# Kernel optimization log

Hardware: AMD Instinct MI355X
Metric: run time of the kernel (lower is better)

## Reference

```python
import jax, jax.numpy as jnp
import numpy as np

N = 10000      # nodes (= num_spatial_nodes)
E = 320000     # edges
IN = 4         # in_channels
HID = 256      # hidden_channels
H1, C1 = 4, 64 # conv1: heads, per-head out (hidden//heads)
EDIM = 1       # edge_feature_size
EPS = 1e-5


def _layernorm(x, g, b):
    mu = jnp.mean(x, axis=-1, keepdims=True)
    var = jnp.mean(jnp.square(x - mu), axis=-1, keepdims=True)
    return (x - mu) / jnp.sqrt(var + EPS) * g + b


def _gatv2(x, src, dst, ea, Wl, bl, Wr, br, We, att, bias, H, C, n):
    # PyG GATv2Conv: lin_l on source, lin_r on target, lin_edge on edge_attr
    xl = (x @ Wl + bl).reshape(n, H, C)
    xr = (x @ Wr + br).reshape(n, H, C)
    ee = (ea @ We).reshape(-1, H, C)
    m = jax.nn.leaky_relu(xl[src] + xr[dst] + ee, 0.2)   # [E', H, C]
    logit = jnp.einsum('ehc,hc->eh', m, att)             # [E', H]
    # segment softmax over incoming edges of each dst node
    mx = jax.ops.segment_max(logit, dst, num_segments=n)
    ex = jnp.exp(logit - mx[dst])
    den = jax.ops.segment_sum(ex, dst, num_segments=n)
    alpha = ex / den[dst]
    out = jax.ops.segment_sum(xl[src] * alpha[:, :, None], dst, num_segments=n)
    return out.reshape(n, H * C) + bias


def setup_inputs() -> dict:
    key = jax.random.key(0)
    ks = jax.random.split(key, 32)
    gl = lambda k, shape, fan: (jax.random.normal(k, shape, jnp.float32) / np.sqrt(fan)).astype(jnp.float32)
    inp = {}
    inp['x'] = jax.random.normal(ks[0], (N, IN), jnp.float32)
    inp['edge_index'] = jax.random.randint(ks[1], (2, E), 0, N, jnp.int32)
    inp['edge_attr'] = jax.random.normal(ks[2], (E, EDIM), jnp.float32)
    # conv1 (heads=4, out=64, concat -> 256)
    inp['Wl1'] = gl(ks[3], (IN, HID), IN);  inp['bl1'] = jnp.zeros((HID,), jnp.float32)
    inp['Wr1'] = gl(ks[4], (IN, HID), IN);  inp['br1'] = jnp.zeros((HID,), jnp.float32)
    inp['We1'] = gl(ks[5], (EDIM, HID), EDIM)
    inp['att1'] = gl(ks[6], (H1, C1), C1)
    inp['bias1'] = jnp.zeros((HID,), jnp.float32)
    inp['g1'] = jnp.ones((HID,), jnp.float32); inp['be1'] = jnp.zeros((HID,), jnp.float32)
    # conv2 (heads=1, out=256)
    inp['Wl2'] = gl(ks[7], (HID, HID), HID); inp['bl2'] = jnp.zeros((HID,), jnp.float32)
    inp['Wr2'] = gl(ks[8], (HID, HID), HID); inp['br2'] = jnp.zeros((HID,), jnp.float32)
    inp['We2'] = gl(ks[9], (EDIM, HID), EDIM)
    inp['att2'] = gl(ks[10], (1, HID), HID)
    inp['bias2'] = jnp.zeros((HID,), jnp.float32)
    inp['g2'] = jnp.ones((HID,), jnp.float32); inp['be2'] = jnp.zeros((HID,), jnp.float32)
    # policy head
    inp['Wp1'] = gl(ks[11], (HID, HID // 2), HID); inp['bp1'] = jnp.zeros((HID // 2,), jnp.float32)
    inp['Wp2'] = gl(ks[12], (HID // 2, IN), HID // 2); inp['bp2'] = jnp.zeros((IN,), jnp.float32)
    return inp


def reference(x, edge_index, edge_attr,
              Wl1, bl1, Wr1, br1, We1, att1, bias1, g1, be1,
              Wl2, bl2, Wr2, br2, We2, att2, bias2, g2, be2,
              Wp1, bp1, Wp2, bp2):
    src, dst = edge_index[0], edge_index[1]
    # add_self_loops with fill_value='mean': loop edge_attr = mean of incoming edge_attr
    deg = jax.ops.segment_sum(jnp.ones((E,), jnp.float32), dst, num_segments=N)
    loop_attr = jax.ops.segment_sum(edge_attr, dst, num_segments=N) / jnp.maximum(deg, 1.0)[:, None]
    ar = jnp.arange(N, dtype=src.dtype)
    src_a = jnp.concatenate([src, ar]); dst_a = jnp.concatenate([dst, ar])
    ea_a = jnp.concatenate([edge_attr, loop_attr], axis=0)
    h = _gatv2(x, src_a, dst_a, ea_a, Wl1, bl1, Wr1, br1, We1, att1, bias1, H1, C1, N)
    h = jax.nn.relu(_layernorm(h, g1, be1))
    h = _gatv2(h, src_a, dst_a, ea_a, Wl2, bl2, Wr2, br2, We2, att2, bias2, 1, HID, N)
    h = jax.nn.relu(_layernorm(h, g2, be2))
    logits = jax.nn.relu(h @ Wp1 + bp1) @ Wp2 + bp2   # [N, IN]
    return jax.nn.softmax(logits.reshape(1, -1), axis=1)
```

## Files before the change

kernel.cpp:

```cpp
#include <hip/hip_runtime.h>
#include <math.h>

#define N_NODES 10000
#define N_EDGES 320000
#define N_AUG   (N_EDGES + N_NODES)
#define HID     256

typedef short short8 __attribute__((ext_vector_type(8)));
typedef float floatx16 __attribute__((ext_vector_type(16)));

static __device__ __forceinline__ unsigned bf16rne(float f) {
  unsigned u = __float_as_uint(f);
  return (u + 0x7FFFu + ((u >> 16) & 1u)) >> 16;
}

__global__ void k_deg(const int* __restrict__ dst, const float* __restrict__ ea,
                      int* __restrict__ deg, float* __restrict__ asum) {
  int e = blockIdx.x * blockDim.x + threadIdx.x;
  if (e < N_EDGES) {
    int d = dst[e];
    atomicAdd(&deg[d], 1);
    atomicAdd(&asum[d], ea[e]);
  }
}

__global__ void __launch_bounds__(256) k_scan(
    const int* __restrict__ deg, const float* __restrict__ asum,
    int* __restrict__ offs, float* __restrict__ lattr) {
  __shared__ int wsum[4];
  int t = threadIdx.x;
  int base = t * 40;
  int s = 0;
  for (int i = 0; i < 40; i++) {
    int n = base + i;
    if (n < N_NODES) s += deg[n] + 1;
  }
  int v = s;
  #pragma unroll
  for (int d = 1; d < 64; d <<= 1) {
    int u = __shfl_up(v, d);
    if ((t & 63) >= d) v += u;
  }
  if ((t & 63) == 63) wsum[t >> 6] = v;
  __syncthreads();
  int wb = 0;
  for (int i = 0; i < (t >> 6); i++) wb += wsum[i];
  int run = wb + v - s;
  for (int i = 0; i < 40; i++) {
    int n = base + i;
    if (n < N_NODES) {
      offs[n] = run;
      int d = deg[n];
      run += d + 1;
      lattr[n] = asum[n] / (float)max(d, 1);
    }
  }
  if (t == 255) offs[N_NODES] = wb + v;
}

__global__ void k_scatter(const int* __restrict__ src, const int* __restrict__ dst,
                          const float* __restrict__ ea, const float* __restrict__ lattr,
                          const int* __restrict__ offs, int* __restrict__ cursor,
                          int2* __restrict__ cpk) {
  int e = blockIdx.x * blockDim.x + threadIdx.x;
  if (e >= N_AUG) return;
  int s, d; float a;
  if (e < N_EDGES) { s = src[e]; d = dst[e]; a = ea[e]; }
  else             { s = e - N_EDGES; d = s; a = lattr[s]; }
  int pos = offs[d] + atomicAdd(&cursor[d], 1);
  cpk[pos] = make_int2(s, __float_as_int(a));
}

__global__ void __launch_bounds__(256) k_cvtw(
    const float* __restrict__ W1, const float* __restrict__ W2,
    unsigned short* __restrict__ Wt) {
  __shared__ float tile[32][33];
  const float* W = blockIdx.z ? W2 : W1;
  int rowoff = blockIdx.z * 256;
  int kb = blockIdx.x * 32, nb = blockIdx.y * 32;
  int t = threadIdx.x;
  int tx = t & 31, ty = t >> 5;
  #pragma unroll
  for (int rep = 0; rep < 4; rep++)
    tile[ty + 8*rep][tx] = W[(kb + ty + 8*rep)*HID + nb + tx];
  __syncthreads();
  #pragma unroll
  for (int rep = 0; rep < 4; rep++) {
    int n = nb + ty + 8*rep;
    Wt[(rowoff + n)*256 + kb + tx] = (unsigned short)bf16rne(tile[tx][ty + 8*rep]);
  }
}

__global__ void __launch_bounds__(256) k_cvtwp(
    const float* __restrict__ Wp1, unsigned short* __restrict__ Wp1t) {
  __shared__ float tile[32][33];
  int kb = blockIdx.x * 32, nb = blockIdx.y * 32;
  int t = threadIdx.x;
  int tx = t & 31, ty = t >> 5;
  #pragma unroll
  for (int rep = 0; rep < 4; rep++)
    tile[ty + 8*rep][tx] = Wp1[(kb + ty + 8*rep)*128 + nb + tx];
  __syncthreads();
  #pragma unroll
  for (int rep = 0; rep < 4; rep++) {
    int n = nb + ty + 8*rep;
    Wp1t[n*256 + kb + tx] = (unsigned short)bf16rne(tile[tx][ty + 8*rep]);
  }
}

#define C1_EDGE(xs, av, l0, l1, l2, l3, p)                                              \
  {                                                                                     \
    l0 = fmaf(xs.x,wl0.x, fmaf(xs.y,wl1.x, fmaf(xs.z,wl2.x, fmaf(xs.w,wl3.x, blv.x)))); \
    l1 = fmaf(xs.x,wl0.y, fmaf(xs.y,wl1.y, fmaf(xs.z,wl2.y, fmaf(xs.w,wl3.y, blv.y)))); \
    l2 = fmaf(xs.x,wl0.z, fmaf(xs.y,wl1.z, fmaf(xs.z,wl2.z, fmaf(xs.w,wl3.z, blv.z)))); \
    l3 = fmaf(xs.x,wl0.w, fmaf(xs.y,wl1.w, fmaf(xs.z,wl2.w, fmaf(xs.w,wl3.w, blv.w)))); \
    float m0 = l0 + fmaf(av, we.x, r4.x); m0 = fmaxf(m0, 0.2f*m0);                      \
    float m1 = l1 + fmaf(av, we.y, r4.y); m1 = fmaxf(m1, 0.2f*m1);                      \
    float m2 = l2 + fmaf(av, we.z, r4.z); m2 = fmaxf(m2, 0.2f*m2);                      \
    float m3 = l3 + fmaf(av, we.w, r4.w); m3 = fmaxf(m3, 0.2f*m3);                      \
    p = m0*at.x + m1*at.y + m2*at.z + m3*at.w;                                          \
  }

#define C1_PROC8()                                                              \
  {                                                                             \
    float4 xA = *(const float4*)&x[eA.x*4];                                     \
    float4 xB = *(const float4*)&x[eB.x*4];                                     \
    float4 xC = *(const float4*)&x[eC.x*4];                                     \
    float4 xD = *(const float4*)&x[eD.x*4];                                     \
    float4 xE = *(const float4*)&x[eE.x*4];                                     \
    float4 xF = *(const float4*)&x[eF.x*4];                                     \
    float4 xG = *(const float4*)&x[eG.x*4];                                     \
    float4 xH = *(const float4*)&x[eH.x*4];                                     \
    float avA = __int_as_float(eA.y), avB = __int_as_float(eB.y);               \
    float avC = __int_as_float(eC.y), avD = __int_as_float(eD.y);               \
    float avE = __int_as_float(eE.y), avF = __int_as_float(eF.y);               \
    float avG = __int_as_float(eG.y), avH = __int_as_float(eH.y);               \
    float lA0,lA1,lA2,lA3,pA, lB0,lB1,lB2,lB3,pB;                               \
    float lC0,lC1,lC2,lC3,pC, lD0,lD1,lD2,lD3,pD;                               \
    float lE0,lE1,lE2,lE3,pE, lF0,lF1,lF2,lF3,pF;                               \
    float lG0,lG1,lG2,lG3,pG, lH0,lH1,lH2,lH3,pH;                               \
    C1_EDGE(xA, avA, lA0,lA1,lA2,lA3, pA);                                      \
    C1_EDGE(xB, avB, lB0,lB1,lB2,lB3, pB);                                      \
    C1_EDGE(xC, avC, lC0,lC1,lC2,lC3, pC);                                      \
    C1_EDGE(xD, avD, lD0,lD1,lD2,lD3, pD);                                      \
    C1_EDGE(xE, avE, lE0,lE1,lE2,lE3, pE);                                      \
    C1_EDGE(xF, avF, lF0,lF1,lF2,lF3, pF);                                      \
    C1_EDGE(xG, avG, lG0,lG1,lG2,lG3, pG);                                      \
    C1_EDGE(xH, avH, lH0,lH1,lH2,lH3, pH);                                      \
    _Pragma("unroll")                                                           \
    for (int msk = 1; msk < 16; msk <<= 1) {                                    \
      pA += __shfl_xor(pA, msk); pB += __shfl_xor(pB, msk);                     \
      pC += __shfl_xor(pC, msk); pD += __shfl_xor(pD, msk);                     \
      pE += __shfl_xor(pE, msk); pF += __shfl_xor(pF, msk);                     \
      pG += __shfl_xor(pG, msk); pH += __shfl_xor(pH, msk);                     \
    }                                                                           \
    float eAx = expf(pA), eBx = expf(pB), eCx = expf(pC), eDx = expf(pD);       \
    float eEx = expf(pE), eFx = expf(pF), eGx = expf(pG), eHx = expf(pH);       \
    D += ((eAx + eBx) + (eCx + eDx)) + ((eEx + eFx) + (eGx + eHx));             \
    a0 = fmaf(eDx, lD0, fmaf(eCx, lC0, fmaf(eBx, lB0, fmaf(eAx, lA0, a0))));    \
    a0 = fmaf(eHx, lH0, fmaf(eGx, lG0, fmaf(eFx, lF0, fmaf(eEx, lE0, a0))));    \
    a1 = fmaf(eDx, lD1, fmaf(eCx, lC1, fmaf(eBx, lB1, fmaf(eAx, lA1, a1))));    \
    a1 = fmaf(eHx, lH1, fmaf(eGx, lG1, fmaf(eFx, lF1, fmaf(eEx, lE1, a1))));    \
    a2 = fmaf(eDx, lD2, fmaf(eCx, lC2, fmaf(eBx, lB2, fmaf(eAx, lA2, a2))));    \
    a2 = fmaf(eHx, lH2, fmaf(eGx, lG2, fmaf(eFx, lF2, fmaf(eEx, lE2, a2))));    \
    a3 = fmaf(eDx, lD3, fmaf(eCx, lC3, fmaf(eBx, lB3, fmaf(eAx, lA3, a3))));    \
    a3 = fmaf(eHx, lH3, fmaf(eGx, lG3, fmaf(eFx, lF3, fmaf(eEx, lE3, a3))));    \
  }

__global__ void __launch_bounds__(256) k_conv1(
    const float* __restrict__ x,
    const float* __restrict__ Wl, const float* __restrict__ bl,
    const float* __restrict__ Wr, const float* __restrict__ br,
    const float* __restrict__ We, const float* __restrict__ att,
    const int* __restrict__ offs, const int2* __restrict__ cpk,
    const float* __restrict__ bias, const float* __restrict__ g,
    const float* __restrict__ be, uint2* __restrict__ h1b) {
  int t = threadIdx.x;
  int n = blockIdx.x * 4 + (t >> 6);
  int c = 4 * (t & 63);

  float4 wl0 = *(const float4*)&Wl[0*HID + c];
  float4 wl1 = *(const float4*)&Wl[1*HID + c];
  float4 wl2 = *(const float4*)&Wl[2*HID + c];
  float4 wl3 = *(const float4*)&Wl[3*HID + c];
  float4 blv = *(const float4*)&bl[c];
  float4 we  = *(const float4*)&We[c];
  float4 at  = *(const float4*)&att[c];

  float4 xn = *(const float4*)&x[n*4];
  float4 r4;
  {
    float4 wr0 = *(const float4*)&Wr[0*HID + c];
    float4 wr1 = *(const float4*)&Wr[1*HID + c];
    float4 wr2 = *(const float4*)&Wr[2*HID + c];
    float4 wr3 = *(const float4*)&Wr[3*HID + c];
    float4 brv = *(const float4*)&br[c];
    r4.x = fmaf(xn.x,wr0.x, fmaf(xn.y,wr1.x, fmaf(xn.z,wr2.x, fmaf(xn.w,wr3.x, brv.x))));
    r4.y = fmaf(xn.x,wr0.y, fmaf(xn.y,wr1.y, fmaf(xn.z,wr2.y, fmaf(xn.w,wr3.y, brv.y))));
    r4.z = fmaf(xn.x,wr0.z, fmaf(xn.y,wr1.z, fmaf(xn.z,wr2.z, fmaf(xn.w,wr3.z, brv.z))));
    r4.w = fmaf(xn.x,wr0.w, fmaf(xn.y,wr1.w, fmaf(xn.z,wr2.w, fmaf(xn.w,wr3.w, brv.w))));
  }

  int js = __builtin_amdgcn_readfirstlane(offs[n]);
  int je = __builtin_amdgcn_readfirstlane(offs[n+1]);

  float D = 0.f, a0 = 0.f, a1 = 0.f, a2 = 0.f, a3 = 0.f;

  int j = js;
  if (j + 7 < je) {
    int2 eA = cpk[j],   eB = cpk[j+1], eC = cpk[j+2], eD = cpk[j+3];
    int2 eE = cpk[j+4], eF = cpk[j+5], eG = cpk[j+6], eH = cpk[j+7];
    for (; j + 7 < je; j += 8) {
      int2 nA = cpk[j+8],  nB = cpk[j+9],  nC = cpk[j+10], nD = cpk[j+11];
      int2 nE = cpk[j+12], nF = cpk[j+13], nG = cpk[j+14], nH = cpk[j+15];
      C1_PROC8();
      eA = nA; eB = nB; eC = nC; eD = nD;
      eE = nE; eF = nF; eG = nG; eH = nH;
    }
  }
  for (; j < je; j++) {
    int2 eA = cpk[j];
    float4 xA = *(const float4*)&x[eA.x*4];
    float avA = __int_as_float(eA.y);
    float lA0,lA1,lA2,lA3,pA;
    C1_EDGE(xA, avA, lA0,lA1,lA2,lA3, pA);
    #pragma unroll
    for (int msk = 1; msk < 16; msk <<= 1) pA += __shfl_xor(pA, msk);
    float eAx = expf(pA);
    D += eAx;
    a0 = fmaf(eAx, lA0, a0);
    a1 = fmaf(eAx, lA1, a1);
    a2 = fmaf(eAx, lA2, a2);
    a3 = fmaf(eAx, lA3, a3);
  }

  float inv = 1.f / D;
  float4 b4 = *(const float4*)&bias[c];
  float o0 = fmaf(a0, inv, b4.x);
  float o1 = fmaf(a1, inv, b4.y);
  float o2 = fmaf(a2, inv, b4.z);
  float o3 = fmaf(a3, inv, b4.w);

  float s = o0 + o1 + o2 + o3;
  #pragma unroll
  for (int msk = 1; msk < 64; msk <<= 1) s += __shfl_xor(s, msk);
  float mu = s * (1.f / 256.f);
  float d0 = o0 - mu, d1 = o1 - mu, d2 = o2 - mu, d3 = o3 - mu;
  float sq = d0*d0 + d1*d1 + d2*d2 + d3*d3;
  #pragma unroll
  for (int msk = 1; msk < 64; msk <<= 1) sq += __shfl_xor(sq, msk);
  float rstd = rsqrtf(sq * (1.f / 256.f) + 1e-5f);
  float4 g4  = *(const float4*)&g[c];
  float4 be4 = *(const float4*)&be[c];
  float oy0 = fmaxf(fmaf(d0 * rstd, g4.x, be4.x), 0.f);
  float oy1 = fmaxf(fmaf(d1 * rstd, g4.y, be4.y), 0.f);
  float oy2 = fmaxf(fmaf(d2 * rstd, g4.z, be4.z), 0.f);
  float oy3 = fmaxf(fmaf(d3 * rstd, g4.w, be4.w), 0.f);
  uint2 pk;
  pk.x = bf16rne(oy0) | (bf16rne(oy1) << 16);
  pk.y = bf16rne(oy2) | (bf16rne(oy3) << 16);
  h1b[n*64 + (t & 63)] = pk;
}

#define C2_LOAD(q, xs)                                  \
  float4 xs;                                            \
  xs.x = __uint_as_float(q.x << 16);                    \
  xs.y = __uint_as_float(q.x & 0xFFFF0000u);            \
  xs.z = __uint_as_float(q.y << 16);                    \
  xs.w = __uint_as_float(q.y & 0xFFFF0000u);

#define C2_EDGE(xs, av, p)                                           \
  {                                                                  \
    float m0 = xs.x + fmaf(av, we.x, r4.x); m0 = fmaxf(m0, 0.2f*m0); \
    float m1 = xs.y + fmaf(av, we.y, r4.y); m1 = fmaxf(m1, 0.2f*m1); \
    float m2 = xs.z + fmaf(av, we.z, r4.z); m2 = fmaxf(m2, 0.2f*m2); \
    float m3 = xs.w + fmaf(av, we.w, r4.w); m3 = fmaxf(m3, 0.2f*m3); \
    p = m0*at.x + m1*at.y + m2*at.z + m3*at.w;                       \
  }

#define C2_PROC8()                                                              \
  {                                                                             \
    uint2 q0 = xlb[e0.x*64 + lane];                                             \
    uint2 q1 = xlb[e1.x*64 + lane];                                             \
    uint2 q2 = xlb[e2.x*64 + lane];                                             \
    uint2 q3 = xlb[e3.x*64 + lane];                                             \
    uint2 q4 = xlb[e4.x*64 + lane];                                             \
    uint2 q5 = xlb[e5.x*64 + lane];                                             \
    uint2 q6 = xlb[e6.x*64 + lane];                                             \
    uint2 q7 = xlb[e7.x*64 + lane];                                             \
    C2_LOAD(q0, xs0); C2_LOAD(q1, xs1); C2_LOAD(q2, xs2); C2_LOAD(q3, xs3);     \
    C2_LOAD(q4, xs4); C2_LOAD(q5, xs5); C2_LOAD(q6, xs6); C2_LOAD(q7, xs7);     \
    float av0 = __int_as_float(e0.y), av1 = __int_as_float(e1.y);               \
    float av2 = __int_as_float(e2.y), av3 = __int_as_float(e3.y);               \
    float av4 = __int_as_float(e4.y), av5 = __int_as_float(e5.y);               \
    float av6 = __int_as_float(e6.y), av7 = __int_as_float(e7.y);               \
    float p0,p1,p2,p3,p4,p5,p6,p7;                                              \
    C2_EDGE(xs0, av0, p0); C2_EDGE(xs1, av1, p1);                               \
    C2_EDGE(xs2, av2, p2); C2_EDGE(xs3, av3, p3);                               \
    C2_EDGE(xs4, av4, p4); C2_EDGE(xs5, av5, p5);                               \
    C2_EDGE(xs6, av6, p6); C2_EDGE(xs7, av7, p7);                               \
    _Pragma("unroll")                                                           \
    for (int msk = 1; msk < 64; msk <<= 1) {                                    \
      p0 += __shfl_xor(p0, msk); p1 += __shfl_xor(p1, msk);                     \
      p2 += __shfl_xor(p2, msk); p3 += __shfl_xor(p3, msk);                     \
      p4 += __shfl_xor(p4, msk); p5 += __shfl_xor(p5, msk);                     \
      p6 += __shfl_xor(p6, msk); p7 += __shfl_xor(p7, msk);                     \
    }                                                                           \
    float x0 = expf(p0), x1 = expf(p1), x2 = expf(p2), x3 = expf(p3);           \
    float x4 = expf(p4), x5 = expf(p5), x6 = expf(p6), x7 = expf(p7);           \
    D += ((x0 + x1) + (x2 + x3)) + ((x4 + x5) + (x6 + x7));                     \
    a0 = fmaf(x3, xs3.x, fmaf(x2, xs2.x, fmaf(x1, xs1.x, fmaf(x0, xs0.x, a0))));\
    a0 = fmaf(x7, xs7.x, fmaf(x6, xs6.x, fmaf(x5, xs5.x, fmaf(x4, xs4.x, a0))));\
    a1 = fmaf(x3, xs3.y, fmaf(x2, xs2.y, fmaf(x1, xs1.y, fmaf(x0, xs0.y, a1))));\
    a1 = fmaf(x7, xs7.y, fmaf(x6, xs6.y, fmaf(x5, xs5.y, fmaf(x4, xs4.y, a1))));\
    a2 = fmaf(x3, xs3.z, fmaf(x2, xs2.z, fmaf(x1, xs1.z, fmaf(x0, xs0.z, a2))));\
    a2 = fmaf(x7, xs7.z, fmaf(x6, xs6.z, fmaf(x5, xs5.z, fmaf(x4, xs4.z, a2))));\
    a3 = fmaf(x3, xs3.w, fmaf(x2, xs2.w, fmaf(x1, xs1.w, fmaf(x0, xs0.w, a3))));\
    a3 = fmaf(x7, xs7.w, fmaf(x6, xs6.w, fmaf(x5, xs5.w, fmaf(x4, xs4.w, a3))));\
  }

__global__ void __launch_bounds__(256) k_conv2(
    const uint2* __restrict__ xlb, const float* __restrict__ xr,
    const int* __restrict__ offs, const int2* __restrict__ cpk,
    const float* __restrict__ We, const float* __restrict__ att,
    const float* __restrict__ bias, const float* __restrict__ g,
    const float* __restrict__ be, uint2* __restrict__ h2b) {
  int t = threadIdx.x;
  int n = blockIdx.x * 4 + (t >> 6);
  int lane = t & 63;
  int c = 4 * lane;
  float4 r4 = *(const float4*)&xr[n*HID + c];
  float4 we = *(const float4*)&We[c];
  float4 at = *(const float4*)&att[c];
  int js = __builtin_amdgcn_readfirstlane(offs[n]);
  int je = __builtin_amdgcn_readfirstlane(offs[n+1]);

  float D = 0.f, a0 = 0.f, a1 = 0.f, a2 = 0.f, a3 = 0.f;

  int j = js;
  if (j + 7 < je) {
    int2 e0 = cpk[j],   e1 = cpk[j+1], e2 = cpk[j+2], e3 = cpk[j+3];
    int2 e4 = cpk[j+4], e5 = cpk[j+5], e6 = cpk[j+6], e7 = cpk[j+7];
    for (; j + 7 < je; j += 8) {
      int2 n0 = cpk[j+8],  n1 = cpk[j+9],  n2 = cpk[j+10], n3 = cpk[j+11];
      int2 n4 = cpk[j+12], n5 = cpk[j+13], n6 = cpk[j+14], n7 = cpk[j+15];
      C2_PROC8();
      e0 = n0; e1 = n1; e2 = n2; e3 = n3;
      e4 = n4; e5 = n5; e6 = n6; e7 = n7;
    }
  }
  for (; j < je; j++) {
    int2 e0 = cpk[j];
    float av0 = __int_as_float(e0.y);
    uint2 q0 = xlb[e0.x*64 + lane];
    C2_LOAD(q0, xs0);
    float p0;
    C2_EDGE(xs0, av0, p0);
    #pragma unroll
    for (int msk = 1; msk < 64; msk <<= 1) p0 += __shfl_xor(p0, msk);
    float x0 = expf(p0);
    D += x0;
    a0 = fmaf(x0, xs0.x, a0);
    a1 = fmaf(x0, xs0.y, a1);
    a2 = fmaf(x0, xs0.z, a2);
    a3 = fmaf(x0, xs0.w, a3);
  }

  float inv = 1.f / D;
  float4 b4 = *(const float4*)&bias[c];
  float o0 = fmaf(a0, inv, b4.x);
  float o1 = fmaf(a1, inv, b4.y);
  float o2 = fmaf(a2, inv, b4.z);
  float o3 = fmaf(a3, inv, b4.w);

  float s = o0 + o1 + o2 + o3;
  #pragma unroll
  for (int msk = 1; msk < 64; msk <<= 1) s += __shfl_xor(s, msk);
  float mu = s * (1.f / 256.f);
  float d0 = o0 - mu, d1 = o1 - mu, d2 = o2 - mu, d3 = o3 - mu;
  float sq = d0*d0 + d1*d1 + d2*d2 + d3*d3;
  #pragma unroll
  for (int msk = 1; msk < 64; msk <<= 1) sq += __shfl_xor(sq, msk);
  float rstd = rsqrtf(sq * (1.f / 256.f) + 1e-5f);
  float4 g4  = *(const float4*)&g[c];
  float4 be4 = *(const float4*)&be[c];
  float oy0 = fmaxf(fmaf(d0 * rstd, g4.x, be4.x), 0.f);
  float oy1 = fmaxf(fmaf(d1 * rstd, g4.y, be4.y), 0.f);
  float oy2 = fmaxf(fmaf(d2 * rstd, g4.z, be4.z), 0.f);
  float oy3 = fmaxf(fmaf(d3 * rstd, g4.w, be4.w), 0.f);
  uint2 pk;
  pk.x = bf16rne(oy0) | (bf16rne(oy1) << 16);
  pk.y = bf16rne(oy2) | (bf16rne(oy3) << 16);
  h2b[n*64 + lane] = pk;
}

__global__ void __launch_bounds__(256) k_gemm_dual(
    const unsigned short* __restrict__ h1b, const unsigned short* __restrict__ Wt,
    const float* __restrict__ b1, const float* __restrict__ b2,
    unsigned short* __restrict__ O1b, float* __restrict__ O2) {
  __shared__ unsigned short A_lds[64][72];
  __shared__ unsigned short W_lds[128][72];
  int t = threadIdx.x;
  int r0 = blockIdx.x * 64;
  int nb0 = blockIdx.y * 128;
  int l = t & 63;
  int wave = t >> 6;
  int wr = wave >> 1, wc = wave & 1;

  floatx16 acc[2] = {{0}, {0}};

  int sar = t >> 2, sak = (t & 3) * 16;
  int arow = min(r0 + sar, N_NODES - 1);
  int swn = t >> 1, swk = (t & 1) * 32;
  const unsigned short* Wrow = &Wt[(nb0 + swn) * 256];

  for (int kb = 0; kb < 256; kb += 64) {
    uint4 av0 = *(const uint4*)&h1b[arow*256 + kb + sak];
    uint4 av1 = *(const uint4*)&h1b[arow*256 + kb + sak + 8];
    uint4 wv0 = *(const uint4*)&Wrow[kb + swk];
    uint4 wv1 = *(const uint4*)&Wrow[kb + swk + 8];
    uint4 wv2 = *(const uint4*)&Wrow[kb + swk + 16];
    uint4 wv3 = *(const uint4*)&Wrow[kb + swk + 24];
    __syncthreads();
    *(uint4*)&A_lds[sar][sak]     = av0;
    *(uint4*)&A_lds[sar][sak + 8] = av1;
    *(uint4*)&W_lds[swn][swk]      = wv0;
    *(uint4*)&W_lds[swn][swk +  8] = wv1;
    *(uint4*)&W_lds[swn][swk + 16] = wv2;
    *(uint4*)&W_lds[swn][swk + 24] = wv3;
    __syncthreads();
    #pragma unroll
    for (int ks = 0; ks < 64; ks += 16) {
      short8 af  = *(const short8*)&A_lds[wr*32 + (l & 31)][ks + 8*(l >> 5)];
      short8 bf0 = *(const short8*)&W_lds[wc*64      + (l & 31)][ks + 8*(l >> 5)];
      short8 bf1 = *(const short8*)&W_lds[wc*64 + 32 + (l & 31)][ks + 8*(l >> 5)];
      acc[0] = __builtin_amdgcn_mfma_f32_32x32x16_bf16(af, bf0, acc[0], 0, 0, 0);
      acc[1] = __builtin_amdgcn_mfma_f32_32x32x16_bf16(af, bf1, acc[1], 0, 0, 0);
    }
  }

  bool isO1 = (nb0 < 256);
  #pragma unroll
  for (int tile = 0; tile < 2; tile++) {
    int col = nb0 + wc*64 + tile*32 + (l & 31);
    float bias = isO1 ? b1[col] : b2[col - 256];
    #pragma unroll
    for (int reg = 0; reg < 16; reg++) {
      int row = (reg & 3) + 8*(reg >> 2) + 4*(l >> 5);
      int r = r0 + wr*32 + row;
      if (r < N_NODES) {
        float v = acc[tile][reg] + bias;
        if (isO1) O1b[r*256 + col] = (unsigned short)bf16rne(v);
        else      O2[r*256 + (col - 256)] = v;
      }
    }
  }
}

__global__ void __launch_bounds__(256) k_policy(
    const unsigned short* __restrict__ h2b, const unsigned short* __restrict__ Wp1t,
    const float* __restrict__ bp1, const float* __restrict__ Wp2,
    const float* __restrict__ bp2, float* __restrict__ elg, float* __restrict__ tot) {
  __shared__ __align__(16) char smembuf[64 * 132 * 4];
  unsigned short* A_lds = (unsigned short*)smembuf;
  unsigned short* W_lds = (unsigned short*)(smembuf + 64*72*2);
  float* hidl = (float*)smembuf;
  __shared__ float wred[4];
  int t = threadIdx.x;
  int r0 = blockIdx.x * 64;
  int l = t & 63;
  int wave = t >> 6;
  int wr = wave >> 1, wc = wave & 1;

  floatx16 acc[2] = {{0}, {0}};

  int sar = t >> 2, sak = (t & 3) * 16;
  int arow = min(r0 + sar, N_NODES - 1);
  int swn = t >> 1, swk = (t & 1) * 32;
  const unsigned short* Wrow = &Wp1t[swn * 256];

  for (int kb = 0; kb < 256; kb += 64) {
    uint4 av0 = *(const uint4*)&h2b[arow*256 + kb + sak];
    uint4 av1 = *(const uint4*)&h2b[arow*256 + kb + sak + 8];
    uint4 wv0 = *(const uint4*)&Wrow[kb + swk];
    uint4 wv1 = *(const uint4*)&Wrow[kb + swk + 8];
    uint4 wv2 = *(const uint4*)&Wrow[kb + swk + 16];
    uint4 wv3 = *(const uint4*)&Wrow[kb + swk + 24];
    __syncthreads();
    *(uint4*)&A_lds[sar*72 + sak]     = av0;
    *(uint4*)&A_lds[sar*72 + sak + 8] = av1;
    *(uint4*)&W_lds[swn*72 + swk]      = wv0;
    *(uint4*)&W_lds[swn*72 + swk +  8] = wv1;
    *(uint4*)&W_lds[swn*72 + swk + 16] = wv2;
    *(uint4*)&W_lds[swn*72 + swk + 24] = wv3;
    __syncthreads();
    #pragma unroll
    for (int ks = 0; ks < 64; ks += 16) {
      short8 af  = *(const short8*)&A_lds[(wr*32 + (l & 31))*72 + ks + 8*(l >> 5)];
      short8 bf0 = *(const short8*)&W_lds[(wc*64      + (l & 31))*72 + ks + 8*(l >> 5)];
      short8 bf1 = *(const short8*)&W_lds[(wc*64 + 32 + (l & 31))*72 + ks + 8*(l >> 5)];
      acc[0] = __builtin_amdgcn_mfma_f32_32x32x16_bf16(af, bf0, acc[0], 0, 0, 0);
      acc[1] = __builtin_amdgcn_mfma_f32_32x32x16_bf16(af, bf1, acc[1], 0, 0, 0);
    }
  }
  __syncthreads();
  #pragma unroll
  for (int tile = 0; tile < 2; tile++) {
    int col = wc*64 + tile*32 + (l & 31);
    float bias = bp1[col];
    #pragma unroll
    for (int reg = 0; reg < 16; reg++) {
      int row = (reg & 3) + 8*(reg >> 2) + 4*(l >> 5) + wr*32;
      hidl[row*132 + col] = fmaxf(acc[tile][reg] + bias, 0.f);
    }
  }
  __syncthreads();
  int nl = t >> 2, i = t & 3;
  float s = bp2[i];
  for (int k = 0; k < 128; k += 4) {
    float4 hv = *(const float4*)&hidl[nl*132 + k];
    s = fmaf(hv.x, Wp2[(k+0)*4 + i],
        fmaf(hv.y, Wp2[(k+1)*4 + i],
        fmaf(hv.z, Wp2[(k+2)*4 + i],
        fmaf(hv.w, Wp2[(k+3)*4 + i], s))));
  }
  int n = r0 + nl;
  float esum = 0.f;
  if (n < N_NODES) {
    float e = expf(s);
    elg[n*4 + i] = e;
    esum = e;
  }
  #pragma unroll
  for (int msk = 1; msk < 64; msk <<= 1) esum += __shfl_xor(esum, msk);
  if ((t & 63) == 0) wred[t >> 6] = esum;
  __syncthreads();
  if (t == 0) atomicAdd(tot, (wred[0] + wred[1]) + (wred[2] + wred[3]));
}

__global__ void __launch_bounds__(1024) k_sm_final(const float* __restrict__ elg,
                                                   const float* __restrict__ tot,
                                                   float* __restrict__ out) {
  int i = blockIdx.x * 1024 + threadIdx.x;
  float inv = 1.f / tot[0];
  if (i < N_NODES * 4) out[i] = elg[i] * inv;
}

extern "C" void kernel_launch(void* const* d_in, const int* in_sizes, int n_in,
                              void* d_out, int out_size, void* d_ws, size_t ws_size,
                              hipStream_t stream) {
  const float* x    = (const float*)d_in[0];
  const int*   ei   = (const int*)  d_in[1];
  const float* ea   = (const float*)d_in[2];
  const float* Wl1  = (const float*)d_in[3];
  const float* bl1  = (const float*)d_in[4];
  const float* Wr1  = (const float*)d_in[5];
  const float* br1  = (const float*)d_in[6];
  const float* We1  = (const float*)d_in[7];
  const float* att1 = (const float*)d_in[8];
  const float* bias1= (const float*)d_in[9];
  const float* g1   = (const float*)d_in[10];
  const float* be1  = (const float*)d_in[11];
  const float* Wl2  = (const float*)d_in[12];
  const float* bl2  = (const float*)d_in[13];
  const float* Wr2  = (const float*)d_in[14];
  const float* br2  = (const float*)d_in[15];
  const float* We2  = (const float*)d_in[16];
  const float* att2 = (const float*)d_in[17];
  const float* bias2= (const float*)d_in[18];
  const float* g2   = (const float*)d_in[19];
  const float* be2  = (const float*)d_in[20];
  const float* Wp1  = (const float*)d_in[21];
  const float* bp1  = (const float*)d_in[22];
  const float* Wp2  = (const float*)d_in[23];
  const float* bp2  = (const float*)d_in[24];
  float* out = (float*)d_out;

  const int* srcp = ei;
  const int* dstp = ei + N_EDGES;

  int*   deg    = (int*)d_ws;
  int*   cursor = deg + 10240;
  float* asum   = (float*)(cursor + 10240);
  float* tot    = asum + 10240;
  int*   offs   = (int*)(tot + 16);
  float* lattr  = (float*)(offs + 10240);
  int2*  cpk    = (int2*)(lattr + 10240);
  unsigned short* h1b = (unsigned short*)(cpk + 330752);
  unsigned short* h2b = h1b;
  unsigned short* xl2bf = h1b + 2560000;
  float* xr2    = (float*)(xl2bf + 2560000);
  float* elg    = xr2 + 2560000;
  unsigned short* Wt   = (unsigned short*)(elg + 40960);
  unsigned short* Wp1t = Wt + 512*256;

  hipMemsetAsync(deg, 0, (3 * 10240 + 16) * sizeof(int), stream);

  k_cvtw   <<<dim3(8, 8, 2), 256, 0, stream>>>(Wl2, Wr2, Wt);
  k_cvtwp  <<<dim3(8, 4), 256, 0, stream>>>(Wp1, Wp1t);
  k_deg    <<<(N_EDGES + 255)/256, 256, 0, stream>>>(dstp, ea, deg, asum);
  k_scan   <<<1, 256, 0, stream>>>(deg, asum, offs, lattr);
  k_scatter<<<(N_AUG + 255)/256, 256, 0, stream>>>(srcp, dstp, ea, lattr, offs,
                                                   cursor, cpk);
  k_conv1  <<<N_NODES/4, 256, 0, stream>>>(x, Wl1, bl1, Wr1, br1, We1, att1,
                                           offs, cpk, bias1, g1, be1, (uint2*)h1b);
  k_gemm_dual<<<dim3(157, 4), 256, 0, stream>>>(h1b, Wt, bl2, br2, xl2bf, xr2);
  k_conv2  <<<N_NODES/4, 256, 0, stream>>>((const uint2*)xl2bf, xr2, offs, cpk,
                                           We2, att2, bias2, g2, be2, (uint2*)h2b);
  k_policy <<<157, 256, 0, stream>>>(h2b, Wp1t, bp1, Wp2, bp2, elg, tot);
  k_sm_final<<<40, 1024, 0, stream>>>(elg, tot, out);
}
```

Measured before the change: 314.4 us.

## Transpose-reduce edge logits and software-pipeline conv2 neighbor gathers

Replaces the eight independent butterfly reductions of per-edge logits with a transposed reduction. Lanes exchange and fold partial sums so that each of the first lanes ends up holding one edge's total, and only one expf per lane is needed before broadcasting the results back. Conv2 also prefetches the next group's edge records and bf16 source-feature rows one iteration ahead, to hide gather latency behind compute. To make those lookahead reads safe, the scatter kernel zero-fills the cpk padding up to its capacity, at the cost of more registers and a longer prologue and epilogue.

Result: faster. 306.2 us (-2.6%).

```diff
diff --git a/kernel.cpp b/kernel.cpp
--- a/kernel.cpp
+++ b/kernel.cpp
@@ -4,6 +4,7 @@
 #define N_NODES 10000
 #define N_EDGES 320000
 #define N_AUG   (N_EDGES + N_NODES)
+#define CPK_CAP 330752
 #define HID     256
 
 typedef short short8 __attribute__((ext_vector_type(8)));
@@ -63,7 +64,10 @@
                           const int* __restrict__ offs, int* __restrict__ cursor,
                           int2* __restrict__ cpk) {
   int e = blockIdx.x * blockDim.x + threadIdx.x;
-  if (e >= N_AUG) return;
+  if (e >= N_AUG) {
+    if (e < CPK_CAP) cpk[e] = make_int2(0, 0);
+    return;
+  }
   int s, d; float a;
   if (e < N_EDGES) { s = src[e]; d = dst[e]; a = ea[e]; }
   else             { s = e - N_EDGES; d = s; a = lattr[s]; }
@@ -147,24 +151,35 @@
     C1_EDGE(xF, avF, lF0,lF1,lF2,lF3, pF);                                      \
     C1_EDGE(xG, avG, lG0,lG1,lG2,lG3, pG);                                      \
     C1_EDGE(xH, avH, lH0,lH1,lH2,lH3, pH);                                      \
-    _Pragma("unroll")                                                           \
-    for (int msk = 1; msk < 16; msk <<= 1) {                                    \
-      pA += __shfl_xor(pA, msk); pB += __shfl_xor(pB, msk);                     \
-      pC += __shfl_xor(pC, msk); pD += __shfl_xor(pD, msk);                     \
-      pE += __shfl_xor(pE, msk); pF += __shfl_xor(pF, msk);                     \
-      pG += __shfl_xor(pG, msk); pH += __shfl_xor(pH, msk);                     \
-    }                                                                           \
-    float eAx = expf(pA), eBx = expf(pB), eCx = expf(pC), eDx = expf(pD);       \
-    float eEx = expf(pE), eFx = expf(pF), eGx = expf(pG), eHx = expf(pH);       \
-    D += ((eAx + eBx) + (eCx + eDx)) + ((eEx + eFx) + (eGx + eHx));             \
-    a0 = fmaf(eDx, lD0, fmaf(eCx, lC0, fmaf(eBx, lB0, fmaf(eAx, lA0, a0))));    \
-    a0 = fmaf(eHx, lH0, fmaf(eGx, lG0, fmaf(eFx, lF0, fmaf(eEx, lE0, a0))));    \
-    a1 = fmaf(eDx, lD1, fmaf(eCx, lC1, fmaf(eBx, lB1, fmaf(eAx, lA1, a1))));    \
-    a1 = fmaf(eHx, lH1, fmaf(eGx, lG1, fmaf(eFx, lF1, fmaf(eEx, lE1, a1))));    \
-    a2 = fmaf(eDx, lD2, fmaf(eCx, lC2, fmaf(eBx, lB2, fmaf(eAx, lA2, a2))));    \
-    a2 = fmaf(eHx, lH2, fmaf(eGx, lG2, fmaf(eFx, lF2, fmaf(eEx, lE2, a2))));    \
-    a3 = fmaf(eDx, lD3, fmaf(eCx, lC3, fmaf(eBx, lB3, fmaf(eAx, lA3, a3))));    \
-    a3 = fmaf(eHx, lH3, fmaf(eGx, lG3, fmaf(eFx, lF3, fmaf(eEx, lE3, a3))));    \
+    float sAB = b1 ? pA : pB, kAB = b1 ? pB : pA;                               \
+    float qAB = kAB + __shfl_xor(sAB, 1);                                       \
+    float sCD = b1 ? pC : pD, kCD = b1 ? pD : pC;                               \
+    float qCD = kCD + __shfl_xor(sCD, 1);                                       \
+    float sEF = b1 ? pE : pF, kEF = b1 ? pF : pE;                               \
+    float qEF = kEF + __shfl_xor(sEF, 1);                                       \
+    float sGH = b1 ? pG : pH, kGH = b1 ? pH : pG;                               \
+    float qGH = kGH + __shfl_xor(sGH, 1);                                       \
+    float u0s = b2 ? qAB : qCD, u0k = b2 ? qCD : qAB;                           \
+    float u0 = u0k + __shfl_xor(u0s, 2);                                        \
+    float u1s = b2 ? qEF : qGH, u1k = b2 ? qGH : qEF;                           \
+    float u1 = u1k + __shfl_xor(u1s, 2);                                        \
+    float vvs = b4 ? u0 : u1, vvk = b4 ? u1 : u0;                               \
+    float vv = vvk + __shfl_xor(vvs, 4);                                        \
+    vv += __shfl_xor(vv, 8);                                                    \
+    float exv = expf(vv);                                                       \
+    float xAe = __shfl(exv, 0, 16), xBe = __shfl(exv, 1, 16);                   \
+    float xCe = __shfl(exv, 2, 16), xDe = __shfl(exv, 3, 16);                   \
+    float xEe = __shfl(exv, 4, 16), xFe = __shfl(exv, 5, 16);                   \
+    float xGe = __shfl(exv, 6, 16), xHe = __shfl(exv, 7, 16);                   \
+    D += ((xAe + xBe) + (xCe + xDe)) + ((xEe + xFe) + (xGe + xHe));             \
+    a0 = fmaf(xDe, lD0, fmaf(xCe, lC0, fmaf(xBe, lB0, fmaf(xAe, lA0, a0))));    \
+    a0 = fmaf(xHe, lH0, fmaf(xGe, lG0, fmaf(xFe, lF0, fmaf(xEe, lE0, a0))));    \
+    a1 = fmaf(xDe, lD1, fmaf(xCe, lC1, fmaf(xBe, lB1, fmaf(xAe, lA1, a1))));    \
+    a1 = fmaf(xHe, lH1, fmaf(xGe, lG1, fmaf(xFe, lF1, fmaf(xEe, lE1, a1))));    \
+    a2 = fmaf(xDe, lD2, fmaf(xCe, lC2, fmaf(xBe, lB2, fmaf(xAe, lA2, a2))));    \
+    a2 = fmaf(xHe, lH2, fmaf(xGe, lG2, fmaf(xFe, lF2, fmaf(xEe, lE2, a2))));    \
+    a3 = fmaf(xDe, lD3, fmaf(xCe, lC3, fmaf(xBe, lB3, fmaf(xAe, lA3, a3))));    \
+    a3 = fmaf(xHe, lH3, fmaf(xGe, lG3, fmaf(xFe, lF3, fmaf(xEe, lE3, a3))));    \
   }
 
 __global__ void __launch_bounds__(256) k_conv1(
@@ -178,6 +193,7 @@
   int t = threadIdx.x;
   int n = blockIdx.x * 4 + (t >> 6);
   int c = 4 * (t & 63);
+  bool b1 = (t & 1) != 0, b2 = (t & 2) != 0, b4 = (t & 4) != 0;
 
   float4 wl0 = *(const float4*)&Wl[0*HID + c];
   float4 wl1 = *(const float4*)&Wl[1*HID + c];
@@ -235,11 +251,11 @@
   }
 
   float inv = 1.f / D;
-  float4 b4 = *(const float4*)&bias[c];
-  float o0 = fmaf(a0, inv, b4.x);
-  float o1 = fmaf(a1, inv, b4.y);
-  float o2 = fmaf(a2, inv, b4.z);
-  float o3 = fmaf(a3, inv, b4.w);
+  float4 b4v = *(const float4*)&bias[c];
+  float o0 = fmaf(a0, inv, b4v.x);
+  float o1 = fmaf(a1, inv, b4v.y);
+  float o2 = fmaf(a2, inv, b4v.z);
+  float o3 = fmaf(a3, inv, b4v.w);
 
   float s = o0 + o1 + o2 + o3;
   #pragma unroll
@@ -280,14 +296,6 @@
 
 #define C2_PROC8()                                                              \
   {                                                                             \
-    uint2 q0 = xlb[e0.x*64 + lane];                                             \
-    uint2 q1 = xlb[e1.x*64 + lane];                                             \
-    uint2 q2 = xlb[e2.x*64 + lane];                                             \
-    uint2 q3 = xlb[e3.x*64 + lane];                                             \
-    uint2 q4 = xlb[e4.x*64 + lane];                                             \
-    uint2 q5 = xlb[e5.x*64 + lane];                                             \
-    uint2 q6 = xlb[e6.x*64 + lane];                                             \
-    uint2 q7 = xlb[e7.x*64 + lane];                                             \
     C2_LOAD(q0, xs0); C2_LOAD(q1, xs1); C2_LOAD(q2, xs2); C2_LOAD(q3, xs3);     \
     C2_LOAD(q4, xs4); C2_LOAD(q5, xs5); C2_LOAD(q6, xs6); C2_LOAD(q7, xs7);     \
     float av0 = __int_as_float(e0.y), av1 = __int_as_float(e1.y);               \
@@ -299,15 +307,28 @@
     C2_EDGE(xs2, av2, p2); C2_EDGE(xs3, av3, p3);                               \
     C2_EDGE(xs4, av4, p4); C2_EDGE(xs5, av5, p5);                               \
     C2_EDGE(xs6, av6, p6); C2_EDGE(xs7, av7, p7);                               \
-    _Pragma("unroll")                                                           \
-    for (int msk = 1; msk < 64; msk <<= 1) {                                    \
-      p0 += __shfl_xor(p0, msk); p1 += __shfl_xor(p1, msk);                     \
-      p2 += __shfl_xor(p2, msk); p3 += __shfl_xor(p3, msk);                     \
-      p4 += __shfl_xor(p4, msk); p5 += __shfl_xor(p5, msk);                     \
-      p6 += __shfl_xor(p6, msk); p7 += __shfl_xor(p7, msk);                     \
-    }                                                                           \
-    float x0 = expf(p0), x1 = expf(p1), x2 = expf(p2), x3 = expf(p3);           \
-    float x4 = expf(p4), x5 = expf(p5), x6 = expf(p6), x7 = expf(p7);           \
+    float sAB = b1 ? p0 : p1, kAB = b1 ? p1 : p0;                               \
+    float qAB = kAB + __shfl_xor(sAB, 1);                                       \
+    float sCD = b1 ? p2 : p3, kCD = b1 ? p3 : p2;                               \
+    float qCD = kCD + __shfl_xor(sCD, 1);                                       \
+    float sEF = b1 ? p4 : p5, kEF = b1 ? p5 : p4;                               \
+    float qEF = kEF + __shfl_xor(sEF, 1);                                       \
+    float sGH = b1 ? p6 : p7, kGH = b1 ? p7 : p6;                               \
+    float qGH = kGH + __shfl_xor(sGH, 1);                                       \
+    float u0s = b2 ? qAB : qCD, u0k = b2 ? qCD : qAB;                           \
+    float u0 = u0k + __shfl_xor(u0s, 2);                                        \
+    float u1s = b2 ? qEF : qGH, u1k = b2 ? qGH : qEF;                           \
+    float u1 = u1k + __shfl_xor(u1s, 2);                                        \
+    float vvs = b4 ? u0 : u1, vvk = b4 ? u1 : u0;                               \
+    float vv = vvk + __shfl_xor(vvs, 4);                                        \
+    vv += __shfl_xor(vv, 8);                                                    \
+    vv += __shfl_xor(vv, 16);                                                   \
+    vv += __shfl_xor(vv, 32);                                                   \
+    float exv = expf(vv);                                                       \
+    float x0 = __shfl(exv, 0), x1 = __shfl(exv, 1);                             \
+    float x2 = __shfl(exv, 2), x3 = __shfl(exv, 3);                             \
+    float x4 = __shfl(exv, 4), x5 = __shfl(exv, 5);                             \
+    float x6 = __shfl(exv, 6), x7 = __shfl(exv, 7);                             \
     D += ((x0 + x1) + (x2 + x3)) + ((x4 + x5) + (x6 + x7));                     \
     a0 = fmaf(x3, xs3.x, fmaf(x2, xs2.x, fmaf(x1, xs1.x, fmaf(x0, xs0.x, a0))));\
     a0 = fmaf(x7, xs7.x, fmaf(x6, xs6.x, fmaf(x5, xs5.x, fmaf(x4, xs4.x, a0))));\
@@ -329,6 +350,7 @@
   int n = blockIdx.x * 4 + (t >> 6);
   int lane = t & 63;
   int c = 4 * lane;
+  bool b1 = (t & 1) != 0, b2 = (t & 2) != 0, b4 = (t & 4) != 0;
   float4 r4 = *(const float4*)&xr[n*HID + c];
   float4 we = *(const float4*)&We[c];
   float4 at = *(const float4*)&att[c];
@@ -338,16 +360,50 @@
   float D = 0.f, a0 = 0.f, a1 = 0.f, a2 = 0.f, a3 = 0.f;
 
   int j = js;
-  if (j + 7 < je) {
+  if (je - js >= 16) {
     int2 e0 = cpk[j],   e1 = cpk[j+1], e2 = cpk[j+2], e3 = cpk[j+3];
     int2 e4 = cpk[j+4], e5 = cpk[j+5], e6 = cpk[j+6], e7 = cpk[j+7];
-    for (; j + 7 < je; j += 8) {
-      int2 n0 = cpk[j+8],  n1 = cpk[j+9],  n2 = cpk[j+10], n3 = cpk[j+11];
-      int2 n4 = cpk[j+12], n5 = cpk[j+13], n6 = cpk[j+14], n7 = cpk[j+15];
+    int2 f0 = cpk[j+8],  f1 = cpk[j+9],  f2 = cpk[j+10], f3 = cpk[j+11];
+    int2 f4 = cpk[j+12], f5 = cpk[j+13], f6 = cpk[j+14], f7 = cpk[j+15];
+    uint2 q0 = xlb[e0.x*64 + lane];
+    uint2 q1 = xlb[e1.x*64 + lane];
+    uint2 q2 = xlb[e2.x*64 + lane];
+    uint2 q3 = xlb[e3.x*64 + lane];
+    uint2 q4 = xlb[e4.x*64 + lane];
+    uint2 q5 = xlb[e5.x*64 + lane];
+    uint2 q6 = xlb[e6.x*64 + lane];
+    uint2 q7 = xlb[e7.x*64 + lane];
+    for (; j + 15 < je; j += 8) {
+      uint2 r0 = xlb[f0.x*64 + lane];
+      uint2 r1 = xlb[f1.x*64 + lane];
+      uint2 r2 = xlb[f2.x*64 + lane];
+      uint2 r3 = xlb[f3.x*64 + lane];
+      uint2 r4_ = xlb[f4.x*64 + lane];
+      uint2 r5 = xlb[f5.x*64 + lane];
+      uint2 r6 = xlb[f6.x*64 + lane];
+      uint2 r7 = xlb[f7.x*64 + lane];
+      int2 g0 = cpk[j+16], g1 = cpk[j+17], g2 = cpk[j+18], g3 = cpk[j+19];
+      int2 g4 = cpk[j+20], g5 = cpk[j+21], g6 = cpk[j+22], g7 = cpk[j+23];
       C2_PROC8();
-      e0 = n0; e1 = n1; e2 = n2; e3 = n3;
-      e4 = n4; e5 = n5; e6 = n6; e7 = n7;
+      e0 = f0; e1 = f1; e2 = f2; e3 = f3; e4 = f4; e5 = f5; e6 = f6; e7 = f7;
+      f0 = g0; f1 = g1; f2 = g2; f3 = g3; f4 = g4; f5 = g5; f6 = g6; f7 = g7;
+      q0 = r0; q1 = r1; q2 = r2; q3 = r3; q4 = r4_; q5 = r5; q6 = r6; q7 = r7;
     }
+    C2_PROC8();
+    j += 8;
+  }
+  for (; j + 7 < je; j += 8) {
+    int2 e0 = cpk[j],   e1 = cpk[j+1], e2 = cpk[j+2], e3 = cpk[j+3];
+    int2 e4 = cpk[j+4], e5 = cpk[j+5], e6 = cpk[j+6], e7 = cpk[j+7];
+    uint2 q0 = xlb[e0.x*64 + lane];
+    uint2 q1 = xlb[e1.x*64 + lane];
+    uint2 q2 = xlb[e2.x*64 + lane];
+    uint2 q3 = xlb[e3.x*64 + lane];
+    uint2 q4 = xlb[e4.x*64 + lane];
+    uint2 q5 = xlb[e5.x*64 + lane];
+    uint2 q6 = xlb[e6.x*64 + lane];
+    uint2 q7 = xlb[e7.x*64 + lane];
+    C2_PROC8();
   }
   for (; j < je; j++) {
     int2 e0 = cpk[j];
@@ -367,11 +423,11 @@
   }
 
   float inv = 1.f / D;
-  float4 b4 = *(const float4*)&bias[c];
-  float o0 = fmaf(a0, inv, b4.x);
-  float o1 = fmaf(a1, inv, b4.y);
-  float o2 = fmaf(a2, inv, b4.z);
-  float o3 = fmaf(a3, inv, b4.w);
+  float4 b4v = *(const float4*)&bias[c];
+  float o0 = fmaf(a0, inv, b4v.x);
+  float o1 = fmaf(a1, inv, b4v.y);
+  float o2 = fmaf(a2, inv, b4v.z);
+  float o3 = fmaf(a3, inv, b4v.w);
 
   float s = o0 + o1 + o2 + o3;
   #pragma unroll
@@ -586,7 +642,7 @@
   int*   offs   = (int*)(tot + 16);
   float* lattr  = (float*)(offs + 10240);
   int2*  cpk    = (int2*)(lattr + 10240);
-  unsigned short* h1b = (unsigned short*)(cpk + 330752);
+  unsigned short* h1b = (unsigned short*)(cpk + CPK_CAP);
   unsigned short* h2b = h1b;
   unsigned short* xl2bf = h1b + 2560000;
   float* xr2    = (float*)(xl2bf + 2560000);
@@ -600,8 +656,8 @@
   k_cvtwp  <<<dim3(8, 4), 256, 0, stream>>>(Wp1, Wp1t);
   k_deg    <<<(N_EDGES + 255)/256, 256, 0, stream>>>(dstp, ea, deg, asum);
   k_scan   <<<1, 256, 0, stream>>>(deg, asum, offs, lattr);
-  k_scatter<<<(N_AUG + 255)/256, 256, 0, stream>>>(srcp, dstp, ea, lattr, offs,
-                                                   cursor, cpk);
+  k_scatter<<<(CPK_CAP + 255)/256, 256, 0, stream>>>(srcp, dstp, ea, lattr, offs,
+                                                     cursor, cpk);
   k_conv1  <<<N_NODES/4, 256, 0, stream>>>(x, Wl1, bl1, Wr1, br1, We1, att1,
                                            offs, cpk, bias1, g1, be1, (uint2*)h1b);
   k_gemm_dual<<<dim3(157, 4), 256, 0, stream>>>(h1b, Wt, bl2, br2, xl2bf, xr2);
```
